# Kernel optimization log

Measured on AMD Instinct MI355X. Metric: run time of the kernel, lower is better.

Reference implementation:

```python
import jax, jax.numpy as jnp
import numpy as np

DILATIONS = [1, 2, 4, 8, 16, 32, 64, 128, 256, 512] * 2  # 20 layers
C = 128      # residual channels
S = 128      # skip channels
K = 3        # kernel size
B = 8        # batch
T = 8192     # timesteps


def _causal_dilated_conv(x, W, b, dilation):
    # x: [B, Cin, T], W: [Cout, Cin, K] -> [B, Cout, T], left-padded (causal)
    pad = (W.shape[-1] - 1) * dilation
    y = jax.lax.conv_general_dilated(
        x, W, window_strides=(1,), padding=[(pad, 0)],
        rhs_dilation=(dilation,), dimension_numbers=('NCH', 'OIH', 'NCH'))
    return y + b[None, :, None]


def setup_inputs() -> dict:
    key = jax.random.key(0)
    ks = jax.random.split(key, 7)
    L = len(DILATIONS)
    scale = 0.05
    x = jax.random.normal(ks[0], (B, C, T), dtype=jnp.float32)
    # gated activation: dilated conv emits 2*C channels (tanh half + sigmoid half)
    Wconv = jax.random.normal(ks[1], (L, 2 * C, C, K), dtype=jnp.float32) * scale
    bconv = jax.random.normal(ks[2], (L, 2 * C), dtype=jnp.float32) * scale
    Wout = jax.random.normal(ks[3], (L, C, C), dtype=jnp.float32) * scale
    bout = jax.random.normal(ks[4], (L, C), dtype=jnp.float32) * scale
    Wskip = jax.random.normal(ks[5], (L, S, C), dtype=jnp.float32) * scale
    bskip = jax.random.normal(ks[6], (L, S), dtype=jnp.float32) * scale
    return {"x": x, "Wconv": Wconv, "bconv": bconv, "Wout": Wout,
            "bout": bout, "Wskip": Wskip, "bskip": bskip}


def reference(x, Wconv, bconv, Wout, bout, Wskip, bskip):
    L = len(DILATIONS)
    skips = []
    for i, d in enumerate(DILATIONS):
        y = _causal_dilated_conv(x, Wconv[i], bconv[i], d)       # [B, 2C, T]
        a, g = jnp.split(y, 2, axis=1)
        z = jnp.tanh(a) * jax.nn.sigmoid(g)                       # gated, [B, C, T]
        skips.append(jnp.einsum('sc,bct->bst', Wskip[i], z) + bskip[i][None, :, None])
        if i < L - 1:
            out = jnp.einsum('oc,bct->bot', Wout[i], z) + bout[i][None, :, None]
        else:
            out = z  # last layer: use_output_transform = False
        x = out + x  # residual add
    return x, jnp.stack(skips)  # ([B,C,T], [L,B,S,T])
```

## Files before the change

### kernel.cpp

```cpp
#include <hip/hip_runtime.h>
#include <hip/hip_bf16.h>

#define L_NUM 20
#define CC 128
#define TB 8192
#define BB 8
#define TT 64

#define NCONV (L_NUM * 3 * 256 * 128)
#define NMAT  (L_NUM * 128 * 128)
#define XN    ((size_t)BB * TB * CC)

typedef __attribute__((ext_vector_type(4))) float f32x4;
typedef __attribute__((ext_vector_type(8))) short bf16x8;
typedef unsigned int u32;

static const int DILS[L_NUM] = {1, 2, 4, 8, 16, 32, 64, 128, 256, 512,
                                1, 2, 4, 8, 16, 32, 64, 128, 256, 512};

__device__ __forceinline__ unsigned short f2b(float f) {
  union { __hip_bfloat16 h; unsigned short u; } cv;
  cv.h = __float2bfloat16(f);
  return cv.u;
}
__device__ __forceinline__ float b2fu(u32 u) {
  union { u32 u; float f; } cv;
  cv.u = u << 16;
  return cv.f;
}

__device__ __forceinline__ int swz(int t, int cbyte) {
  return (t * 256 + cbyte) ^ ((t & 7) << 4);
}

__device__ __forceinline__ void gload16(const void* g, void* l) {
  __builtin_amdgcn_global_load_lds(
      (const __attribute__((address_space(1))) u32*)g,
      (__attribute__((address_space(3))) u32*)l, 16, 0, 0);
}

__global__ void prep_kernel(const float* __restrict__ Wconv,
                            const float* __restrict__ Wout,
                            const float* __restrict__ Wskip,
                            unsigned short* __restrict__ wc,
                            unsigned short* __restrict__ wo,
                            unsigned short* __restrict__ wsk,
                            unsigned short* __restrict__ zp) {
  int i = blockIdx.x * 256 + threadIdx.x;
  if (i < 128) zp[i] = 0;
  if (i < NCONV) {
    int c = i & 127;
    int o = (i >> 7) & 255;
    int lk = i >> 15;
    int k = lk % 3;
    int l = lk / 3;
    wc[i] = f2b(Wconv[((size_t)(l * 256 + o) * 128 + c) * 3 + k]);
  }
  if (i < NMAT) {
    wo[i]  = f2b(Wout[i]);
    wsk[i] = f2b(Wskip[i]);
  }
}

__global__ __launch_bounds__(256) void x0t_kernel(const float* __restrict__ x0,
                                                  unsigned short* __restrict__ hi,
                                                  unsigned short* __restrict__ lo) {
  __shared__ unsigned short Hs[TT * CC], Ls[TT * CC];
  const int tid = threadIdx.x, lane = tid & 63, w = tid >> 6;
  const int b = blockIdx.y, t0 = blockIdx.x * TT;
  const float* xb = x0 + (size_t)b * CC * TB;
#pragma unroll
  for (int it = 0; it < 8; ++it) {
    int c0 = it * 16 + w * 4;
    u32 hu[4], lu[4];
#pragma unroll
    for (int i2 = 0; i2 < 4; ++i2) {
      float v = xb[(size_t)(c0 + i2) * TB + t0 + lane];
      unsigned short h = f2b(v);
      hu[i2] = h;
      lu[i2] = f2b(v - b2fu(h));
    }
    uint2 hp, lp;
    hp.x = hu[0] | (hu[1] << 16); hp.y = hu[2] | (hu[3] << 16);
    lp.x = lu[0] | (lu[1] << 16); lp.y = lu[2] | (lu[3] << 16);
    *reinterpret_cast<uint2*>(reinterpret_cast<char*>(Hs) + swz(lane, c0 * 2)) = hp;
    *reinterpret_cast<uint2*>(reinterpret_cast<char*>(Ls) + swz(lane, c0 * 2)) = lp;
  }
  __syncthreads();
  unsigned short* hb = hi + ((size_t)b * TB + t0) * CC;
  unsigned short* lb = lo + ((size_t)b * TB + t0) * CC;
#pragma unroll
  for (int it = 0; it < 4; ++it) {
    int o = it * 4096 + tid * 16;
    int t = o >> 8;
    int cb = (o & 255) ^ ((t & 7) << 4);
    *reinterpret_cast<f32x4*>(reinterpret_cast<char*>(hb) + (size_t)t * 256 + cb) =
        *reinterpret_cast<f32x4*>(reinterpret_cast<char*>(Hs) + o);
    *reinterpret_cast<f32x4*>(reinterpret_cast<char*>(lb) + (size_t)t * 256 + cb) =
        *reinterpret_cast<f32x4*>(reinterpret_cast<char*>(Ls) + o);
  }
}

__global__ __launch_bounds__(256, 2) void layer_kernel(
    const unsigned short* __restrict__ hin,
    unsigned short* __restrict__ hout,
    unsigned short* __restrict__ lob,
    const unsigned short* __restrict__ zpage,
    const unsigned short* __restrict__ Wc,
    const float* __restrict__ bconv,
    const unsigned short* __restrict__ Wo,
    const float* __restrict__ bout,
    const unsigned short* __restrict__ Wsk,
    const float* __restrict__ bskip,
    float* __restrict__ skipo,
    float* __restrict__ fxout,
    int dil, int last) {
  __shared__ unsigned short Xs[3][TT * CC];

  const int tid = threadIdx.x;
  const int lane = tid & 63;
  const int w = tid >> 6;
  const int lo16 = lane & 15;
  const int hi4 = lane >> 4;
  const int b = blockIdx.y;
  const int t0 = blockIdx.x * TT;

  const unsigned short* hb = hin + (size_t)b * TB * CC;

#pragma unroll
  for (int k = 0; k < 3; ++k) {
    int tbase = t0 + (k - 2) * dil;
#pragma unroll
    for (int i = 0; i < 4; ++i) {
      int o = w * 4096 + i * 1024 + lane * 16;
      int tl = o >> 8;
      int cb = (o & 255) ^ ((tl & 7) << 4);
      int tg = tbase + tl;
      const char* src = (tg >= 0)
          ? (reinterpret_cast<const char*>(hb + (size_t)tg * CC) + cb)
          : (reinterpret_cast<const char*>(zpage) + cb);
      gload16(src, reinterpret_cast<char*>(&Xs[k][0]) + w * 4096 + i * 1024);
    }
  }
  __syncthreads();

  f32x4 zero4 = {0.f, 0.f, 0.f, 0.f};
  f32x4 accA[2][4], accG[2][4];
#pragma unroll
  for (int r = 0; r < 2; ++r)
#pragma unroll
    for (int j = 0; j < 4; ++j) { accA[r][j] = zero4; accG[r][j] = zero4; }

#pragma unroll
  for (int k = 0; k < 3; ++k) {
    const unsigned short* Wk = Wc + k * 256 * 128;
#pragma unroll
    for (int kk = 0; kk < 4; ++kk) {
      int c0 = kk * 32 + hi4 * 8;
      bf16x8 aA0 = *reinterpret_cast<const bf16x8*>(Wk + (w * 32 + lo16) * 128 + c0);
      bf16x8 aA1 = *reinterpret_cast<const bf16x8*>(Wk + (w * 32 + 16 + lo16) * 128 + c0);
      bf16x8 aG0 = *reinterpret_cast<const bf16x8*>(Wk + (128 + w * 32 + lo16) * 128 + c0);
      bf16x8 aG1 = *reinterpret_cast<const bf16x8*>(Wk + (128 + w * 32 + 16 + lo16) * 128 + c0);
#pragma unroll
      for (int j = 0; j < 4; ++j) {
        bf16x8 bx = *reinterpret_cast<const bf16x8*>(
            reinterpret_cast<const char*>(&Xs[k][0]) + swz(j * 16 + lo16, c0 * 2));
        accA[0][j] = __builtin_amdgcn_mfma_f32_16x16x32_bf16(aA0, bx, accA[0][j], 0, 0, 0);
        accA[1][j] = __builtin_amdgcn_mfma_f32_16x16x32_bf16(aA1, bx, accA[1][j], 0, 0, 0);
        accG[0][j] = __builtin_amdgcn_mfma_f32_16x16x32_bf16(aG0, bx, accG[0][j], 0, 0, 0);
        accG[1][j] = __builtin_amdgcn_mfma_f32_16x16x32_bf16(aG1, bx, accG[1][j], 0, 0, 0);
      }
    }
  }

  float bcA[2][4], bcG[2][4];
#pragma unroll
  for (int r = 0; r < 2; ++r)
#pragma unroll
    for (int reg = 0; reg < 4; ++reg) {
      int row = w * 32 + r * 16 + hi4 * 4 + reg;
      bcA[r][reg] = bconv[row];
      bcG[r][reg] = bconv[128 + row];
    }

  __syncthreads();

#pragma unroll
  for (int r = 0; r < 2; ++r) {
#pragma unroll
    for (int j = 0; j < 4; ++j) {
      u32 zu[4];
#pragma unroll
      for (int reg = 0; reg < 4; ++reg) {
        float a = accA[r][j][reg] + bcA[r][reg];
        float g = accG[r][j][reg] + bcG[r][reg];
        float ea = __expf(2.f * a);
        float th = (ea - 1.f) / (ea + 1.f);
        float sg = 1.f / (1.f + __expf(-g));
        zu[reg] = f2b(th * sg);
      }
      uint2 p;
      p.x = zu[0] | (zu[1] << 16);
      p.y = zu[2] | (zu[3] << 16);
      int t = j * 16 + lo16;
      int cB = w * 32 + r * 16 + hi4 * 4;
      *reinterpret_cast<uint2*>(reinterpret_cast<char*>(&Xs[0][0]) + swz(t, cB * 2)) = p;
    }
  }
  __syncthreads();

  f32x4 accS[2][4], accO[2][4];
#pragma unroll
  for (int r = 0; r < 2; ++r)
#pragma unroll
    for (int j = 0; j < 4; ++j) { accS[r][j] = zero4; accO[r][j] = zero4; }

#pragma unroll
  for (int kk = 0; kk < 4; ++kk) {
    int c0 = kk * 32 + hi4 * 8;
    bf16x8 aS0 = *reinterpret_cast<const bf16x8*>(Wsk + (w * 32 + lo16) * 128 + c0);
    bf16x8 aS1 = *reinterpret_cast<const bf16x8*>(Wsk + (w * 32 + 16 + lo16) * 128 + c0);
    bf16x8 aO0 = *reinterpret_cast<const bf16x8*>(Wo + (w * 32 + lo16) * 128 + c0);
    bf16x8 aO1 = *reinterpret_cast<const bf16x8*>(Wo + (w * 32 + 16 + lo16) * 128 + c0);
#pragma unroll
    for (int j = 0; j < 4; ++j) {
      bf16x8 bx = *reinterpret_cast<const bf16x8*>(
          reinterpret_cast<const char*>(&Xs[0][0]) + swz(j * 16 + lo16, c0 * 2));
      accS[0][j] = __builtin_amdgcn_mfma_f32_16x16x32_bf16(aS0, bx, accS[0][j], 0, 0, 0);
      accS[1][j] = __builtin_amdgcn_mfma_f32_16x16x32_bf16(aS1, bx, accS[1][j], 0, 0, 0);
      accO[0][j] = __builtin_amdgcn_mfma_f32_16x16x32_bf16(aO0, bx, accO[0][j], 0, 0, 0);
      accO[1][j] = __builtin_amdgcn_mfma_f32_16x16x32_bf16(aO1, bx, accO[1][j], 0, 0, 0);
    }
  }

  float bsk[2][4], bo[2][4];
#pragma unroll
  for (int r = 0; r < 2; ++r)
#pragma unroll
    for (int reg = 0; reg < 4; ++reg) {
      int row = w * 32 + r * 16 + hi4 * 4 + reg;
      bsk[r][reg] = bskip[row];
      bo[r][reg] = bout[row];
    }

  __syncthreads();

  float* skb = skipo + (size_t)b * CC * TB;
  float* fxb = fxout + (size_t)b * CC * TB;
  const unsigned short* lrow = lob + ((size_t)b * TB + t0) * CC;

#pragma unroll
  for (int r = 0; r < 2; ++r) {
#pragma unroll
    for (int j = 0; j < 4; ++j) {
      int t = j * 16 + lo16;
      int cB = w * 32 + r * 16 + hi4 * 4;
      uint2 hp = *reinterpret_cast<const uint2*>(
          reinterpret_cast<const char*>(&Xs[2][0]) + swz(t, cB * 2));
      uint2 lp = *reinterpret_cast<const uint2*>(
          reinterpret_cast<const char*>(lrow) + (size_t)t * 256 + cB * 2);
      u32 hu[4] = {hp.x & 0xffffu, hp.x >> 16, hp.y & 0xffffu, hp.y >> 16};
      u32 lu[4] = {lp.x & 0xffffu, lp.x >> 16, lp.y & 0xffffu, lp.y >> 16};
      float vout[4];
      if (last) {
        uint2 zp = *reinterpret_cast<const uint2*>(
            reinterpret_cast<const char*>(&Xs[0][0]) + swz(t, cB * 2));
        u32 zu[4] = {zp.x & 0xffffu, zp.x >> 16, zp.y & 0xffffu, zp.y >> 16};
#pragma unroll
        for (int reg = 0; reg < 4; ++reg)
          vout[reg] = b2fu(zu[reg]) + b2fu(hu[reg]) + b2fu(lu[reg]);
      } else {
#pragma unroll
        for (int reg = 0; reg < 4; ++reg)
          vout[reg] = accO[r][j][reg] + bo[r][reg] + b2fu(hu[reg]) + b2fu(lu[reg]);
      }
#pragma unroll
      for (int reg = 0; reg < 4; ++reg)
        skb[(size_t)(cB + reg) * TB + t0 + t] = accS[r][j][reg] + bsk[r][reg];
      if (last) {
#pragma unroll
        for (int reg = 0; reg < 4; ++reg)
          fxb[(size_t)(cB + reg) * TB + t0 + t] = vout[reg];
      } else {
        u32 ho[4], lo4[4];
#pragma unroll
        for (int reg = 0; reg < 4; ++reg) {
          unsigned short h = f2b(vout[reg]);
          ho[reg] = h;
          lo4[reg] = f2b(vout[reg] - b2fu(h));
        }
        uint2 hq, lq;
        hq.x = ho[0] | (ho[1] << 16); hq.y = ho[2] | (ho[3] << 16);
        lq.x = lo4[0] | (lo4[1] << 16); lq.y = lo4[2] | (lo4[3] << 16);
        *reinterpret_cast<uint2*>(reinterpret_cast<char*>(&Xs[0][0]) + swz(t, cB * 2)) = hq;
        *reinterpret_cast<uint2*>(reinterpret_cast<char*>(&Xs[1][0]) + swz(t, cB * 2)) = lq;
      }
    }
  }

  if (!last) {
    __syncthreads();
    unsigned short* hrow = hout + ((size_t)b * TB + t0) * CC;
    unsigned short* lwrow = lob + ((size_t)b * TB + t0) * CC;
#pragma unroll
    for (int it = 0; it < 4; ++it) {
      int o = it * 4096 + tid * 16;
      int t = o >> 8;
      int cb = (o & 255) ^ ((t & 7) << 4);
      *reinterpret_cast<f32x4*>(reinterpret_cast<char*>(hrow) + (size_t)t * 256 + cb) =
          *reinterpret_cast<f32x4*>(reinterpret_cast<char*>(&Xs[0][0]) + o);
      *reinterpret_cast<f32x4*>(reinterpret_cast<char*>(lwrow) + (size_t)t * 256 + cb) =
          *reinterpret_cast<f32x4*>(reinterpret_cast<char*>(&Xs[1][0]) + o);
    }
  }
}

extern "C" void kernel_launch(void* const* d_in, const int* in_sizes, int n_in,
                              void* d_out, int out_size, void* d_ws, size_t ws_size,
                              hipStream_t stream) {
  const float* x0    = (const float*)d_in[0];
  const float* Wconv = (const float*)d_in[1];
  const float* bconv = (const float*)d_in[2];
  const float* Wout  = (const float*)d_in[3];
  const float* bout  = (const float*)d_in[4];
  const float* Wskip = (const float*)d_in[5];
  const float* bskip = (const float*)d_in[6];

  unsigned short* wc  = (unsigned short*)d_ws;
  unsigned short* wo  = wc + NCONV;
  unsigned short* wsk = wo + NMAT;
  unsigned short* zp  = wsk + NMAT;
  unsigned short* hiA = zp + 128;
  unsigned short* lob = hiA + XN;

  float* fx = (float*)d_out;
  float* skips = fx + XN;
  unsigned short* hiB = (unsigned short*)d_out;

  prep_kernel<<<(NCONV + 255) / 256, 256, 0, stream>>>(Wconv, Wout, Wskip, wc, wo, wsk, zp);
  x0t_kernel<<<dim3(TB / TT, BB), 256, 0, stream>>>(x0, hiB, lob);

  for (int l = 0; l < L_NUM; ++l) {
    const unsigned short* hin = (l % 2 == 0) ? hiB : hiA;
    unsigned short* hout      = (l % 2 == 0) ? hiA : hiB;
    layer_kernel<<<dim3(TB / TT, BB), 256, 0, stream>>>(
        hin, hout, lob, zp,
        wc + (size_t)l * 3 * 256 * 128, bconv + (size_t)l * 256,
        wo + (size_t)l * 128 * 128, bout + (size_t)l * 128,
        wsk + (size_t)l * 128 * 128, bskip + (size_t)l * 128,
        skips + (size_t)l * XN, fx,
        DILS[l], l == L_NUM - 1 ? 1 : 0);
  }
}
```

Baseline: 1.050 ms.

## Load conv operands directly from global, shrink LDS to one buffer, remap blocks per XCD

```diff
diff --git a/kernel.cpp b/kernel.cpp
--- a/kernel.cpp
+++ b/kernel.cpp
@@ -31,12 +31,6 @@
 
 __device__ __forceinline__ int swz(int t, int cbyte) {
   return (t * 256 + cbyte) ^ ((t & 7) << 4);
-}
-
-__device__ __forceinline__ void gload16(const void* g, void* l) {
-  __builtin_amdgcn_global_load_lds(
-      (const __attribute__((address_space(1))) u32*)g,
-      (__attribute__((address_space(3))) u32*)l, 16, 0, 0);
 }
 
 __global__ void prep_kernel(const float* __restrict__ Wconv,
@@ -93,15 +87,16 @@
   for (int it = 0; it < 4; ++it) {
     int o = it * 4096 + tid * 16;
     int t = o >> 8;
-    int cb = (o & 255) ^ ((t & 7) << 4);
-    *reinterpret_cast<f32x4*>(reinterpret_cast<char*>(hb) + (size_t)t * 256 + cb) =
-        *reinterpret_cast<f32x4*>(reinterpret_cast<char*>(Hs) + o);
-    *reinterpret_cast<f32x4*>(reinterpret_cast<char*>(lb) + (size_t)t * 256 + cb) =
-        *reinterpret_cast<f32x4*>(reinterpret_cast<char*>(Ls) + o);
-  }
-}
-
-__global__ __launch_bounds__(256, 2) void layer_kernel(
+    int cl = o & 255;
+    int li = t * 256 + (cl ^ ((t & 7) << 4));
+    *reinterpret_cast<f32x4*>(reinterpret_cast<char*>(hb) + (size_t)t * 256 + cl) =
+        *reinterpret_cast<f32x4*>(reinterpret_cast<char*>(Hs) + li);
+    *reinterpret_cast<f32x4*>(reinterpret_cast<char*>(lb) + (size_t)t * 256 + cl) =
+        *reinterpret_cast<f32x4*>(reinterpret_cast<char*>(Ls) + li);
+  }
+}
+
+__global__ __launch_bounds__(256, 3) void layer_kernel(
     const unsigned short* __restrict__ hin,
     unsigned short* __restrict__ hout,
     unsigned short* __restrict__ lob,
@@ -115,34 +110,31 @@
     float* __restrict__ skipo,
     float* __restrict__ fxout,
     int dil, int last) {
-  __shared__ unsigned short Xs[3][TT * CC];
+  __shared__ unsigned short Zs[TT * CC];
 
   const int tid = threadIdx.x;
   const int lane = tid & 63;
   const int w = tid >> 6;
   const int lo16 = lane & 15;
   const int hi4 = lane >> 4;
-  const int b = blockIdx.y;
-  const int t0 = blockIdx.x * TT;
+
+  int p = blockIdx.x + (blockIdx.y << 7);
+  int xcd = p & 7, ii = p >> 3;
+  int bx = (xcd << 4) | (ii >> 3);
+  int b = ii & 7;
+  int t0 = bx * TT;
 
   const unsigned short* hb = hin + (size_t)b * TB * CC;
 
-#pragma unroll
-  for (int k = 0; k < 3; ++k) {
-    int tbase = t0 + (k - 2) * dil;
-#pragma unroll
-    for (int i = 0; i < 4; ++i) {
-      int o = w * 4096 + i * 1024 + lane * 16;
-      int tl = o >> 8;
-      int cb = (o & 255) ^ ((tl & 7) << 4);
-      int tg = tbase + tl;
-      const char* src = (tg >= 0)
-          ? (reinterpret_cast<const char*>(hb + (size_t)tg * CC) + cb)
-          : (reinterpret_cast<const char*>(zpage) + cb);
-      gload16(src, reinterpret_cast<char*>(&Xs[k][0]) + w * 4096 + i * 1024);
-    }
-  }
-  __syncthreads();
+  float bcA[2][4], bcG[2][4];
+#pragma unroll
+  for (int r = 0; r < 2; ++r)
+#pragma unroll
+    for (int reg = 0; reg < 4; ++reg) {
+      int row = w * 32 + r * 16 + hi4 * 4 + reg;
+      bcA[r][reg] = bconv[row];
+      bcG[r][reg] = bconv[128 + row];
+    }
 
   f32x4 zero4 = {0.f, 0.f, 0.f, 0.f};
   f32x4 accA[2][4], accG[2][4];
@@ -154,6 +146,13 @@
 #pragma unroll
   for (int k = 0; k < 3; ++k) {
     const unsigned short* Wk = Wc + k * 256 * 128;
+    int tb = t0 - (2 - k) * dil;
+    const unsigned short* rowp[4];
+#pragma unroll
+    for (int j = 0; j < 4; ++j) {
+      int tg = tb + j * 16 + lo16;
+      rowp[j] = (tg >= 0) ? (hb + (size_t)tg * CC) : zpage;
+    }
 #pragma unroll
     for (int kk = 0; kk < 4; ++kk) {
       int c0 = kk * 32 + hi4 * 8;
@@ -163,27 +162,14 @@
       bf16x8 aG1 = *reinterpret_cast<const bf16x8*>(Wk + (128 + w * 32 + 16 + lo16) * 128 + c0);
 #pragma unroll
       for (int j = 0; j < 4; ++j) {
-        bf16x8 bx = *reinterpret_cast<const bf16x8*>(
-            reinterpret_cast<const char*>(&Xs[k][0]) + swz(j * 16 + lo16, c0 * 2));
-        accA[0][j] = __builtin_amdgcn_mfma_f32_16x16x32_bf16(aA0, bx, accA[0][j], 0, 0, 0);
-        accA[1][j] = __builtin_amdgcn_mfma_f32_16x16x32_bf16(aA1, bx, accA[1][j], 0, 0, 0);
-        accG[0][j] = __builtin_amdgcn_mfma_f32_16x16x32_bf16(aG0, bx, accG[0][j], 0, 0, 0);
-        accG[1][j] = __builtin_amdgcn_mfma_f32_16x16x32_bf16(aG1, bx, accG[1][j], 0, 0, 0);
+        bf16x8 bx8 = *reinterpret_cast<const bf16x8*>(rowp[j] + c0);
+        accA[0][j] = __builtin_amdgcn_mfma_f32_16x16x32_bf16(aA0, bx8, accA[0][j], 0, 0, 0);
+        accA[1][j] = __builtin_amdgcn_mfma_f32_16x16x32_bf16(aA1, bx8, accA[1][j], 0, 0, 0);
+        accG[0][j] = __builtin_amdgcn_mfma_f32_16x16x32_bf16(aG0, bx8, accG[0][j], 0, 0, 0);
+        accG[1][j] = __builtin_amdgcn_mfma_f32_16x16x32_bf16(aG1, bx8, accG[1][j], 0, 0, 0);
       }
     }
   }
-
-  float bcA[2][4], bcG[2][4];
-#pragma unroll
-  for (int r = 0; r < 2; ++r)
-#pragma unroll
-    for (int reg = 0; reg < 4; ++reg) {
-      int row = w * 32 + r * 16 + hi4 * 4 + reg;
-      bcA[r][reg] = bconv[row];
-      bcG[r][reg] = bconv[128 + row];
-    }
-
-  __syncthreads();
 
 #pragma unroll
   for (int r = 0; r < 2; ++r) {
@@ -199,15 +185,36 @@
         float sg = 1.f / (1.f + __expf(-g));
         zu[reg] = f2b(th * sg);
       }
-      uint2 p;
-      p.x = zu[0] | (zu[1] << 16);
-      p.y = zu[2] | (zu[3] << 16);
+      uint2 pz;
+      pz.x = zu[0] | (zu[1] << 16);
+      pz.y = zu[2] | (zu[3] << 16);
       int t = j * 16 + lo16;
       int cB = w * 32 + r * 16 + hi4 * 4;
-      *reinterpret_cast<uint2*>(reinterpret_cast<char*>(&Xs[0][0]) + swz(t, cB * 2)) = p;
+      *reinterpret_cast<uint2*>(reinterpret_cast<char*>(Zs) + swz(t, cB * 2)) = pz;
     }
   }
   __syncthreads();
+
+  const unsigned short* lb = lob + (size_t)b * TB * CC;
+  uint2 hres[2][4], lres[2][4];
+  float bsk[2][4], bo[2][4];
+#pragma unroll
+  for (int r = 0; r < 2; ++r)
+#pragma unroll
+    for (int j = 0; j < 4; ++j) {
+      int t = t0 + j * 16 + lo16;
+      int cB = w * 32 + r * 16 + hi4 * 4;
+      hres[r][j] = *reinterpret_cast<const uint2*>(hb + (size_t)t * CC + cB);
+      lres[r][j] = *reinterpret_cast<const uint2*>(lb + (size_t)t * CC + cB);
+    }
+#pragma unroll
+  for (int r = 0; r < 2; ++r)
+#pragma unroll
+    for (int reg = 0; reg < 4; ++reg) {
+      int row = w * 32 + r * 16 + hi4 * 4 + reg;
+      bsk[r][reg] = bskip[row];
+      bo[r][reg] = bout[row];
+    }
 
   f32x4 accS[2][4], accO[2][4];
 #pragma unroll
@@ -224,30 +231,19 @@
     bf16x8 aO1 = *reinterpret_cast<const bf16x8*>(Wo + (w * 32 + 16 + lo16) * 128 + c0);
 #pragma unroll
     for (int j = 0; j < 4; ++j) {
-      bf16x8 bx = *reinterpret_cast<const bf16x8*>(
-          reinterpret_cast<const char*>(&Xs[0][0]) + swz(j * 16 + lo16, c0 * 2));
-      accS[0][j] = __builtin_amdgcn_mfma_f32_16x16x32_bf16(aS0, bx, accS[0][j], 0, 0, 0);
-      accS[1][j] = __builtin_amdgcn_mfma_f32_16x16x32_bf16(aS1, bx, accS[1][j], 0, 0, 0);
-      accO[0][j] = __builtin_amdgcn_mfma_f32_16x16x32_bf16(aO0, bx, accO[0][j], 0, 0, 0);
-      accO[1][j] = __builtin_amdgcn_mfma_f32_16x16x32_bf16(aO1, bx, accO[1][j], 0, 0, 0);
-    }
-  }
-
-  float bsk[2][4], bo[2][4];
-#pragma unroll
-  for (int r = 0; r < 2; ++r)
-#pragma unroll
-    for (int reg = 0; reg < 4; ++reg) {
-      int row = w * 32 + r * 16 + hi4 * 4 + reg;
-      bsk[r][reg] = bskip[row];
-      bo[r][reg] = bout[row];
-    }
-
-  __syncthreads();
+      bf16x8 bz = *reinterpret_cast<const bf16x8*>(
+          reinterpret_cast<const char*>(Zs) + swz(j * 16 + lo16, c0 * 2));
+      accS[0][j] = __builtin_amdgcn_mfma_f32_16x16x32_bf16(aS0, bz, accS[0][j], 0, 0, 0);
+      accS[1][j] = __builtin_amdgcn_mfma_f32_16x16x32_bf16(aS1, bz, accS[1][j], 0, 0, 0);
+      accO[0][j] = __builtin_amdgcn_mfma_f32_16x16x32_bf16(aO0, bz, accO[0][j], 0, 0, 0);
+      accO[1][j] = __builtin_amdgcn_mfma_f32_16x16x32_bf16(aO1, bz, accO[1][j], 0, 0, 0);
+    }
+  }
 
   float* skb = skipo + (size_t)b * CC * TB;
   float* fxb = fxout + (size_t)b * CC * TB;
-  const unsigned short* lrow = lob + ((size_t)b * TB + t0) * CC;
+  unsigned short* hrow = hout + (size_t)b * TB * CC;
+  unsigned short* lrow = lob + (size_t)b * TB * CC;
 
 #pragma unroll
   for (int r = 0; r < 2; ++r) {
@@ -255,62 +251,36 @@
     for (int j = 0; j < 4; ++j) {
       int t = j * 16 + lo16;
       int cB = w * 32 + r * 16 + hi4 * 4;
-      uint2 hp = *reinterpret_cast<const uint2*>(
-          reinterpret_cast<const char*>(&Xs[2][0]) + swz(t, cB * 2));
-      uint2 lp = *reinterpret_cast<const uint2*>(
-          reinterpret_cast<const char*>(lrow) + (size_t)t * 256 + cB * 2);
-      u32 hu[4] = {hp.x & 0xffffu, hp.x >> 16, hp.y & 0xffffu, hp.y >> 16};
-      u32 lu[4] = {lp.x & 0xffffu, lp.x >> 16, lp.y & 0xffffu, lp.y >> 16};
-      float vout[4];
-      if (last) {
-        uint2 zp = *reinterpret_cast<const uint2*>(
-            reinterpret_cast<const char*>(&Xs[0][0]) + swz(t, cB * 2));
-        u32 zu[4] = {zp.x & 0xffffu, zp.x >> 16, zp.y & 0xffffu, zp.y >> 16};
-#pragma unroll
-        for (int reg = 0; reg < 4; ++reg)
-          vout[reg] = b2fu(zu[reg]) + b2fu(hu[reg]) + b2fu(lu[reg]);
-      } else {
-#pragma unroll
-        for (int reg = 0; reg < 4; ++reg)
-          vout[reg] = accO[r][j][reg] + bo[r][reg] + b2fu(hu[reg]) + b2fu(lu[reg]);
-      }
+      u32 hu[4] = {hres[r][j].x & 0xffffu, hres[r][j].x >> 16,
+                   hres[r][j].y & 0xffffu, hres[r][j].y >> 16};
+      u32 lu[4] = {lres[r][j].x & 0xffffu, lres[r][j].x >> 16,
+                   lres[r][j].y & 0xffffu, lres[r][j].y >> 16};
 #pragma unroll
       for (int reg = 0; reg < 4; ++reg)
         skb[(size_t)(cB + reg) * TB + t0 + t] = accS[r][j][reg] + bsk[r][reg];
       if (last) {
+        uint2 zp2 = *reinterpret_cast<const uint2*>(
+            reinterpret_cast<const char*>(Zs) + swz(t, cB * 2));
+        u32 zu[4] = {zp2.x & 0xffffu, zp2.x >> 16, zp2.y & 0xffffu, zp2.y >> 16};
 #pragma unroll
         for (int reg = 0; reg < 4; ++reg)
-          fxb[(size_t)(cB + reg) * TB + t0 + t] = vout[reg];
+          fxb[(size_t)(cB + reg) * TB + t0 + t] =
+              b2fu(zu[reg]) + b2fu(hu[reg]) + b2fu(lu[reg]);
       } else {
         u32 ho[4], lo4[4];
 #pragma unroll
         for (int reg = 0; reg < 4; ++reg) {
-          unsigned short h = f2b(vout[reg]);
+          float v = accO[r][j][reg] + bo[r][reg] + b2fu(hu[reg]) + b2fu(lu[reg]);
+          unsigned short h = f2b(v);
           ho[reg] = h;
-          lo4[reg] = f2b(vout[reg] - b2fu(h));
+          lo4[reg] = f2b(v - b2fu(h));
         }
         uint2 hq, lq;
         hq.x = ho[0] | (ho[1] << 16); hq.y = ho[2] | (ho[3] << 16);
         lq.x = lo4[0] | (lo4[1] << 16); lq.y = lo4[2] | (lo4[3] << 16);
-        *reinterpret_cast<uint2*>(reinterpret_cast<char*>(&Xs[0][0]) + swz(t, cB * 2)) = hq;
-        *reinterpret_cast<uint2*>(reinterpret_cast<char*>(&Xs[1][0]) + swz(t, cB * 2)) = lq;
+        *reinterpret_cast<uint2*>(hrow + (size_t)(t0 + t) * CC + cB) = hq;
+        *reinterpret_cast<uint2*>(lrow + (size_t)(t0 + t) * CC + cB) = lq;
       }
-    }
-  }
-
-  if (!last) {
-    __syncthreads();
-    unsigned short* hrow = hout + ((size_t)b * TB + t0) * CC;
-    unsigned short* lwrow = lob + ((size_t)b * TB + t0) * CC;
-#pragma unroll
-    for (int it = 0; it < 4; ++it) {
-      int o = it * 4096 + tid * 16;
-      int t = o >> 8;
-      int cb = (o & 255) ^ ((t & 7) << 4);
-      *reinterpret_cast<f32x4*>(reinterpret_cast<char*>(hrow) + (size_t)t * 256 + cb) =
-          *reinterpret_cast<f32x4*>(reinterpret_cast<char*>(&Xs[0][0]) + o);
-      *reinterpret_cast<f32x4*>(reinterpret_cast<char*>(lwrow) + (size_t)t * 256 + cb) =
-          *reinterpret_cast<f32x4*>(reinterpret_cast<char*>(&Xs[1][0]) + o);
     }
   }
 }
```

Result: slower. 1.479 ms (+40.9%).
